# Performance work log

Hardware: AMD Instinct MI355X
Metric: run time of the kernel (lower is better)

## Reference

```python
import jax, jax.numpy as jnp
import numpy as np

EMB_DIM = 32
UID_TGT = 200000
IID_TGT = 50000
BATCH = 128
TOPK = 50000          # hardcoded inside test_source_free branch
TARGET_LABEL = 4.0    # module-level target rating constant


def setup_inputs() -> dict:
    key = jax.random.key(0)
    k1, k2, k3, k4, k5 = jax.random.split(key, 5)
    # x: column 0 = item id (stored as float, like the torch code), cols 1: = src_rate_pre
    iid = jax.random.randint(k1, (BATCH,), 0, IID_TGT).astype(jnp.float32)
    src_rate = jax.random.normal(k2, (BATCH, EMB_DIM), dtype=jnp.float32)
    x = jnp.concatenate([iid[:, None], src_rate], axis=1)  # [B, 1+D]
    uid_weight = 0.1 * jax.random.normal(k3, (UID_TGT, EMB_DIM), dtype=jnp.float32)
    iid_weight = 0.1 * jax.random.normal(k4, (IID_TGT, EMB_DIM), dtype=jnp.float32)
    rp_weight = 0.1 * jax.random.normal(k5, (EMB_DIM, EMB_DIM), dtype=jnp.float32)
    return {"x": x, "uid_weight": uid_weight, "iid_weight": iid_weight, "rp_weight": rp_weight}


def reference(x, uid_weight, iid_weight, rp_weight):
    # === stage == 'test_source_free' ===
    iid = x[:, 0].astype(jnp.int32)                     # [B]
    iid_emb = iid_weight[iid]                           # [B, D] item embedding gather
    src_rate_pre = x[:, 1:] @ rp_weight.T               # [B, D] Linear(emb,emb,bias=False)
    # |uid_emb . src_rate - target|  (torch: [U,B]; here kept [B,U])
    predict_rate = jnp.abs(src_rate_pre @ uid_weight.T - TARGET_LABEL)  # [B, U]
    # torch: full sort ascending + take first TOPK  ==  bottom-TOPK per row
    _, topk_idx = jax.lax.top_k(-predict_rate, TOPK)    # [B, TOPK]
    # voted rating = <selected user emb, item emb>; compute all dots once,
    # then gather (same math as gathering [B,TOPK,D] embeddings and dotting).
    all_scores = iid_emb @ uid_weight.T                 # [B, U]
    voted_rating = jnp.take_along_axis(all_scores, topk_idx, axis=1)  # [B, TOPK]
    mean_rating = jnp.mean(voted_rating, axis=1)        # [B]
    return mean_rating
```

## Files before the change

### kernel.cpp

```cpp
#include <hip/hip_runtime.h>
#include <hip/hip_bf16.h>
#include <stdint.h>

#define EMB    32
#define BATCH  128
#define NU     200000
#define KSEL   50000
#define XCOLS  33
#define SLOTS  64
#define NBLK   256

#define OFF_SPRE   0
#define OFF_IIDE   16384
#define OFF_GHIST  32768
#define OFF_BASE16 163840
#define OFF_PREFIX 164352
#define OFF_M2     164864
#define OFF_EQ     165376
#define OFF_CAND   173568
#define OFF_PART   173568
#define PART_BYTES ((size_t)NBLK * 128 * 256 * 4)

__global__ void prep_kernel(const float* __restrict__ x,
                            const float* __restrict__ iid_w,
                            const float* __restrict__ rp,
                            const float* __restrict__ uid,
                            float* __restrict__ s_pre,
                            float* __restrict__ iid_emb,
                            uint32_t* __restrict__ base16) {
    const int b = blockIdx.x;
    const int t = threadIdx.x;
    __shared__ float xr[EMB];
    if (t < EMB) xr[t] = x[b * XCOLS + 1 + t];
    __syncthreads();
    if (t < EMB) {
        float acc = 0.f;
        #pragma unroll
        for (int k = 0; k < EMB; ++k) acc += xr[k] * rp[t * EMB + k];
        s_pre[b * EMB + t] = acc;
    } else {
        const int d = t - EMB;
        const int iid = (int)x[b * XCOLS];
        iid_emb[b * EMB + d] = iid_w[(size_t)iid * EMB + d];
    }
    __syncthreads();
    if (t == 0) {
        float dot = 0.f;
        #pragma unroll
        for (int k = 0; k < EMB; ++k) dot += s_pre[b * EMB + k] * uid[k];
        const uint32_t bits = __float_as_uint(fabsf(dot - 4.0f));
        const uint32_t hi = bits >> 16;
        base16[b] = (hi > 128u) ? (hi - 128u) : 0u;
    }
}

__global__ void zero_kernel(uint32_t* __restrict__ p, int n) {
    int i = blockIdx.x * blockDim.x + threadIdx.x;
    if (i < n) p[i] = 0u;
}

template <bool PART>
__global__ __launch_bounds__(1024)
__attribute__((amdgpu_waves_per_eu(4, 4)))
void sweep1_kernel(const float* __restrict__ s_pre,
                   const float* __restrict__ uid,
                   const uint32_t* __restrict__ base16,
                   uint32_t* __restrict__ gout,
                   int jchunk) {
    extern __shared__ uint32_t hist[];
    const int t  = threadIdx.x;
    const int b  = t & 127;
    const int jl = t >> 7;
    for (int i = t; i < 128 * 257; i += 1024) hist[i] = 0u;
    float s[EMB];
    #pragma unroll
    for (int d = 0; d < EMB; ++d) s[d] = s_pre[b * EMB + d];
    const uint32_t base = base16[b];
    __syncthreads();

    const int j0 = blockIdx.x * jchunk;
    const int jend = min(j0 + jchunk, NU);
    int j = j0 + jl;
    for (; j + 8 < jend; j += 16) {
        const int ju = __builtin_amdgcn_readfirstlane(j);
        const float* up0 = uid + (size_t)ju * EMB;
        const float* up1 = up0 + 8 * EMB;
        float d0 = 0.f, d1 = 0.f;
        #pragma unroll
        for (int k = 0; k < EMB; ++k) {
            d0 += s[k] * up0[k];
            d1 += s[k] * up1[k];
        }
        const uint32_t bits0 = __float_as_uint(fabsf(d0 - 4.0f));
        const uint32_t bits1 = __float_as_uint(fabsf(d1 - 4.0f));
        int dg0 = (int)(bits0 >> 16) - (int)base; dg0 = dg0 < 0 ? 0 : (dg0 > 255 ? 255 : dg0);
        int dg1 = (int)(bits1 >> 16) - (int)base; dg1 = dg1 < 0 ? 0 : (dg1 > 255 ? 255 : dg1);
        atomicAdd(&hist[b * 257 + dg0], 1u);
        atomicAdd(&hist[b * 257 + dg1], 1u);
    }
    for (; j < jend; j += 8) {
        const int ju = __builtin_amdgcn_readfirstlane(j);
        const float* up0 = uid + (size_t)ju * EMB;
        float d0 = 0.f;
        #pragma unroll
        for (int k = 0; k < EMB; ++k) d0 += s[k] * up0[k];
        const uint32_t bits0 = __float_as_uint(fabsf(d0 - 4.0f));
        int dg0 = (int)(bits0 >> 16) - (int)base; dg0 = dg0 < 0 ? 0 : (dg0 > 255 ? 255 : dg0);
        atomicAdd(&hist[b * 257 + dg0], 1u);
    }
    __syncthreads();
    if (PART) {
        uint32_t* part = gout + (size_t)blockIdx.x * 32768;
        for (int i = t * 4; i < 32768; i += 4096) {
            const int row = i >> 8, d = i & 255;
            uint4 v;
            v.x = hist[row * 257 + d + 0];
            v.y = hist[row * 257 + d + 1];
            v.z = hist[row * 257 + d + 2];
            v.w = hist[row * 257 + d + 3];
            *(uint4*)(part + i) = v;
        }
    } else {
        for (int i = t; i < 128 * 256; i += 1024) {
            const uint32_t c = hist[(i >> 8) * 257 + (i & 255)];
            if (c) atomicAdd(&gout[i], c);
        }
    }
}

__global__ void scan1_kernel(const uint32_t* __restrict__ ghist,
                             const uint32_t* __restrict__ base16,
                             uint32_t* __restrict__ prefix16,
                             uint32_t* __restrict__ m2) {
    const int b = threadIdx.x;
    uint32_t cum = 0, before = 0;
    int c1 = 255;
    for (int d = 0; d < 256; ++d) {
        const uint32_t c = ghist[b * 256 + d];
        if (cum + c >= (uint32_t)KSEL) { c1 = d; before = cum; break; }
        cum += c;
        if (d == 255) before = cum;
    }
    prefix16[b] = base16[b] + (uint32_t)c1;
    m2[b] = (uint32_t)KSEL - before;
}

__global__ __launch_bounds__(256)
void scan1_part_kernel(const uint32_t* __restrict__ part,
                       const uint32_t* __restrict__ base16,
                       uint32_t* __restrict__ prefix16,
                       uint32_t* __restrict__ m2) {
    const int row = blockIdx.x;
    const int t = threadIdx.x;
    __shared__ uint32_t h[256];
    uint32_t a0 = 0, a1 = 0, a2 = 0, a3 = 0;
    const uint32_t* p = part + (size_t)row * 256 + t;
    for (int g = 0; g < NBLK; g += 4) {
        a0 += p[(size_t)(g + 0) * 32768];
        a1 += p[(size_t)(g + 1) * 32768];
        a2 += p[(size_t)(g + 2) * 32768];
        a3 += p[(size_t)(g + 3) * 32768];
    }
    h[t] = a0 + a1 + a2 + a3;
    __syncthreads();
    if (t == 0) {
        uint32_t cum = 0, before = 0; int c1 = 255;
        for (int d = 0; d < 256; ++d) {
            const uint32_t c = h[d];
            if (cum + c >= (uint32_t)KSEL) { c1 = d; before = cum; break; }
            cum += c;
            if (d == 255) before = cum;
        }
        prefix16[row] = base16[row] + (uint32_t)c1;
        m2[row] = (uint32_t)KSEL - before;
    }
}

__global__ __launch_bounds__(1024)
__attribute__((amdgpu_waves_per_eu(4, 4)))
void sweep2_kernel(const float* __restrict__ s_pre,
                   const float* __restrict__ iid_emb,
                   const float* __restrict__ uid,
                   const uint32_t* __restrict__ prefix16,
                   uint32_t* __restrict__ eq_cnt,
                   float* __restrict__ sum_part,
                   uint64_t* __restrict__ cand,
                   int cap, int jchunk) {
    extern __shared__ char smem2[];
    uint64_t* lcand = (uint64_t*)smem2;
    uint32_t* lcnt  = (uint32_t*)(smem2 + 65536);
    uint32_t* lbase = (uint32_t*)(smem2 + 66048);
    float*    sums  = (float*)(smem2 + 66560);
    const int t  = threadIdx.x;
    const int b  = t & 127;
    const int jl = t >> 7;
    if (t < 128) lcnt[t] = 0u;
    float s[EMB], e[EMB];
    #pragma unroll
    for (int d = 0; d < EMB; ++d) { s[d] = s_pre[b*EMB+d]; e[d] = iid_emb[b*EMB+d]; }
    const uint32_t pfx = prefix16[b];
    __syncthreads();

    const int j0 = blockIdx.x * jchunk;
    const int jend = min(j0 + jchunk, NU);
    float local = 0.f;
    int j = j0 + jl;
    for (; j + 8 < jend; j += 16) {
        const int ju = __builtin_amdgcn_readfirstlane(j);
        const float* up0 = uid + (size_t)ju * EMB;
        const float* up1 = up0 + 8 * EMB;
        float d0 = 0.f, v0 = 0.f, d1 = 0.f, v1 = 0.f;
        #pragma unroll
        for (int k = 0; k < EMB; ++k) {
            const float u0 = up0[k], u1 = up1[k];
            d0 += s[k] * u0;  v0 += e[k] * u0;
            d1 += s[k] * u1;  v1 += e[k] * u1;
        }
        const uint32_t bits0 = __float_as_uint(fabsf(d0 - 4.0f));
        const uint32_t bits1 = __float_as_uint(fabsf(d1 - 4.0f));
        const uint32_t hi0 = bits0 >> 16, hi1 = bits1 >> 16;
        local += (hi0 < pfx) ? v0 : 0.f;
        local += (hi1 < pfx) ? v1 : 0.f;
        if (hi0 == pfx) {
            const uint32_t pos = atomicAdd(&lcnt[b], 1u);
            const uint64_t pk = ((uint64_t)bits0 << 32) | (uint32_t)j;
            if (pos < (uint32_t)SLOTS) lcand[b * SLOTS + pos] = pk;
            else {
                const uint32_t g = atomicAdd(&eq_cnt[b * 16], 1u);
                if (g < (uint32_t)cap) cand[(size_t)b * cap + g] = pk;
            }
        }
        if (hi1 == pfx) {
            const uint32_t pos = atomicAdd(&lcnt[b], 1u);
            const uint64_t pk = ((uint64_t)bits1 << 32) | (uint32_t)(j + 8);
            if (pos < (uint32_t)SLOTS) lcand[b * SLOTS + pos] = pk;
            else {
                const uint32_t g = atomicAdd(&eq_cnt[b * 16], 1u);
                if (g < (uint32_t)cap) cand[(size_t)b * cap + g] = pk;
            }
        }
    }
    for (; j < jend; j += 8) {
        const int ju = __builtin_amdgcn_readfirstlane(j);
        const float* up0 = uid + (size_t)ju * EMB;
        float d0 = 0.f, v0 = 0.f;
        #pragma unroll
        for (int k = 0; k < EMB; ++k) {
            const float u0 = up0[k];
            d0 += s[k] * u0;  v0 += e[k] * u0;
        }
        const uint32_t bits0 = __float_as_uint(fabsf(d0 - 4.0f));
        const uint32_t hi0 = bits0 >> 16;
        local += (hi0 < pfx) ? v0 : 0.f;
        if (hi0 == pfx) {
            const uint32_t pos = atomicAdd(&lcnt[b], 1u);
            const uint64_t pk = ((uint64_t)bits0 << 32) | (uint32_t)j;
            if (pos < (uint32_t)SLOTS) lcand[b * SLOTS + pos] = pk;
            else {
                const uint32_t g = atomicAdd(&eq_cnt[b * 16], 1u);
                if (g < (uint32_t)cap) cand[(size_t)b * cap + g] = pk;
            }
        }
    }
    sums[t] = local;
    __syncthreads();
    if (t < 128) {
        float acc = 0.f;
        #pragma unroll
        for (int l = 0; l < 8; ++l) acc += sums[l * 128 + t];
        sum_part[blockIdx.x * 128 + t] = acc;
        const uint32_t n = min(lcnt[t], (uint32_t)SLOTS);
        lbase[t] = atomicAdd(&eq_cnt[t * 16], n);
    }
    __syncthreads();
    for (int i = t; i < 128 * SLOTS; i += 1024) {
        const int bb = i >> 6;
        const int sl = i & 63;
        if (sl < (int)min(lcnt[bb], (uint32_t)SLOTS)) {
            const uint32_t p = lbase[bb] + (uint32_t)sl;
            if (p < (uint32_t)cap) cand[(size_t)bb * cap + p] = lcand[i];
        }
    }
}

__global__ __launch_bounds__(256)
void final_kernel(const float* __restrict__ iid_emb,
                  const float* __restrict__ uid,
                  const uint32_t* __restrict__ m2_,
                  const uint32_t* __restrict__ eq_cnt,
                  const float* __restrict__ sum_part,
                  const uint64_t* __restrict__ cand,
                  int cap, float* __restrict__ out) {
    const int b = blockIdx.x;
    const int t = threadIdx.x;
    __shared__ float red[256];
    __shared__ uint32_t hist[256];
    __shared__ float e[EMB];
    __shared__ uint32_t tie[128];
    __shared__ uint32_t tiecnt, sc2, sm3, sc3, sm4;
    __shared__ float sbelow;
    if (t < EMB) e[t] = iid_emb[b * EMB + t];
    if (t == 0) tiecnt = 0u;
    hist[t] = 0u;
    red[t] = sum_part[t * 128 + b];
    __syncthreads();
    for (int s = 128; s > 0; s >>= 1) { if (t < s) red[t] += red[t + s]; __syncthreads(); }
    if (t == 0) sbelow = red[0];
    __syncthreads();

    const uint32_t ec = eq_cnt[b * 16];
    const int cnt = (int)(ec < (uint32_t)cap ? ec : (uint32_t)cap);
    const uint64_t* cb = cand + (size_t)b * cap;

    for (int i = t; i < cnt; i += 256) {
        const uint32_t low16 = (uint32_t)(cb[i] >> 32) & 0xFFFFu;
        atomicAdd(&hist[low16 >> 8], 1u);
    }
    __syncthreads();
    if (t == 0) {
        const uint32_t m2v = m2_[b];
        uint32_t cum = 0, before = 0; int c2 = 255;
        for (int d = 0; d < 256; ++d) {
            const uint32_t c = hist[d];
            if (cum + c >= m2v) { c2 = d; before = cum; break; }
            cum += c;
        }
        sc2 = (uint32_t)c2; sm3 = m2v - before;
    }
    __syncthreads();
    const uint32_t c2 = sc2;
    hist[t] = 0u;
    __syncthreads();

    for (int i = t; i < cnt; i += 256) {
        const uint32_t low16 = (uint32_t)(cb[i] >> 32) & 0xFFFFu;
        if ((low16 >> 8) == c2) atomicAdd(&hist[low16 & 255u], 1u);
    }
    __syncthreads();
    if (t == 0) {
        const uint32_t m3 = sm3;
        uint32_t cum = 0, before = 0; int c3 = 255;
        for (int d = 0; d < 256; ++d) {
            const uint32_t c = hist[d];
            if (cum + c >= m3) { c3 = d; before = cum; break; }
            cum += c;
        }
        sc3 = (uint32_t)c3; sm4 = m3 - before;
    }
    __syncthreads();
    const uint32_t T16 = (c2 << 8) | sc3;

    float local = 0.f;
    for (int i = t; i < cnt; i += 256) {
        const uint64_t cv = cb[i];
        const uint32_t low16 = (uint32_t)(cv >> 32) & 0xFFFFu;
        if (low16 < T16) {
            const uint32_t j = (uint32_t)cv;
            const float4* u4 = (const float4*)(uid + (size_t)j * EMB);
            float dv = 0.f;
            #pragma unroll
            for (int q = 0; q < 8; ++q) {
                float4 u = u4[q];
                dv += e[4*q+0]*u.x + e[4*q+1]*u.y + e[4*q+2]*u.z + e[4*q+3]*u.w;
            }
            local += dv;
        } else if (low16 == T16) {
            const uint32_t pos = atomicAdd(&tiecnt, 1u);
            if (pos < 128u) tie[pos] = (uint32_t)cv;
        }
    }
    red[t] = local;
    __syncthreads();
    for (int s = 128; s > 0; s >>= 1) { if (t < s) red[t] += red[t + s]; __syncthreads(); }
    if (t == 0) {
        int tc = (int)(tiecnt < 128u ? tiecnt : 128u);
        for (int i = 1; i < tc; ++i) {
            const uint32_t v = tie[i]; int k = i - 1;
            while (k >= 0 && tie[k] > v) { tie[k+1] = tie[k]; --k; }
            tie[k+1] = v;
        }
        const int m4 = (int)sm4;
        float tsum = 0.f;
        for (int i = 0; i < m4 && i < tc; ++i) {
            const uint32_t j = tie[i];
            float dv = 0.f;
            for (int d = 0; d < EMB; ++d) dv += e[d] * uid[(size_t)j * EMB + d];
            tsum += dv;
        }
        out[b] = (sbelow + red[0] + tsum) / (float)KSEL;
    }
}

extern "C" void kernel_launch(void* const* d_in, const int* in_sizes, int n_in,
                              void* d_out, int out_size, void* d_ws, size_t ws_size,
                              hipStream_t stream) {
    const float* x     = (const float*)d_in[0];
    const float* uid   = (const float*)d_in[1];
    const float* iid_w = (const float*)d_in[2];
    const float* rp    = (const float*)d_in[3];
    float* out = (float*)d_out;

    char* ws = (char*)d_ws;
    float*    s_pre    = (float*)(ws + OFF_SPRE);
    float*    iid_emb  = (float*)(ws + OFF_IIDE);
    uint32_t* ghist    = (uint32_t*)(ws + OFF_GHIST);
    float*    sum_part = (float*)(ws + OFF_GHIST);
    uint32_t* base16   = (uint32_t*)(ws + OFF_BASE16);
    uint32_t* prefix16 = (uint32_t*)(ws + OFF_PREFIX);
    uint32_t* m2       = (uint32_t*)(ws + OFF_M2);
    uint32_t* eq_cnt   = (uint32_t*)(ws + OFF_EQ);
    uint32_t* part     = (uint32_t*)(ws + OFF_PART);

    const size_t off_cand2 = OFF_PART + PART_BYTES;
    const bool use_part = ws_size >= off_cand2 + (size_t)128 * 8 * 4096;

    uint64_t* cand;
    int cap;
    if (use_part) {
        cand = (uint64_t*)(ws + off_cand2);
        long long cap_ll = ((long long)ws_size - (long long)off_cand2) / (128LL * 8LL);
        cap = (int)(cap_ll > 16384 ? 16384 : cap_ll);
    } else {
        cand = (uint64_t*)(ws + OFF_CAND);
        long long cap_ll = ((long long)ws_size - OFF_CAND) / (128LL * 8LL);
        cap = (int)(cap_ll > 16384 ? 16384 : (cap_ll < 1 ? 1 : cap_ll));
    }

    {
        const int n = (OFF_CAND - OFF_GHIST) / 4;
        zero_kernel<<<(n + 255) / 256, 256, 0, stream>>>((uint32_t*)(ws + OFF_GHIST), n);
    }
    prep_kernel<<<BATCH, 64, 0, stream>>>(x, iid_w, rp, uid, s_pre, iid_emb, base16);

    const int JC = 782;
    if (use_part) {
        sweep1_kernel<true><<<NBLK, 1024, 128 * 257 * 4, stream>>>(s_pre, uid, base16, part, JC);
        scan1_part_kernel<<<BATCH, 256, 0, stream>>>(part, base16, prefix16, m2);
    } else {
        sweep1_kernel<false><<<NBLK, 1024, 128 * 257 * 4, stream>>>(s_pre, uid, base16, ghist, JC);
        scan1_kernel<<<1, 128, 0, stream>>>(ghist, base16, prefix16, m2);
    }

    sweep2_kernel<<<NBLK, 1024, 65536 + 512 + 512 + 4096, stream>>>(s_pre, iid_emb, uid,
                                                                    prefix16, eq_cnt, sum_part,
                                                                    cand, cap, JC);

    final_kernel<<<BATCH, 256, 0, stream>>>(iid_emb, uid, m2, eq_cnt, sum_part,
                                            cand, cap, out);
}
```

Before: 241.8 us.

## Split each dot product across four lanes with float4 loads and swizzle reductions

Both sweep kernels now give each (batch, user) dot product to four lanes. Each lane loads 8 floats as two float4s and the partial sums are combined with ds_swizzle, replacing per-thread 32-float register arrays and scalar row loads. This cuts register pressure so the fixed waves_per_eu hint can be dropped, and it makes uid reads coalesced vector loads. sweep2 now runs on 512 blocks when the partial-histogram workspace is available, reusing that buffer for sum_part, and the final kernel reduces over a variable number of block partials. Costs include the extra swizzle steps, three of four lanes idling during histogram and candidate updates, and shared-memory atomics for the per-row sums.

```diff
diff --git a/kernel.cpp b/kernel.cpp
--- a/kernel.cpp
+++ b/kernel.cpp
@@ -8,7 +8,8 @@
 #define KSEL   50000
 #define XCOLS  33
 #define SLOTS  64
-#define NBLK   256
+#define NBLK1  256
+#define NBLK2  512
 
 #define OFF_SPRE   0
 #define OFF_IIDE   16384
@@ -19,7 +20,17 @@
 #define OFF_EQ     165376
 #define OFF_CAND   173568
 #define OFF_PART   173568
-#define PART_BYTES ((size_t)NBLK * 128 * 256 * 4)
+#define PART_BYTES ((size_t)NBLK1 * 128 * 256 * 4)
+
+__device__ __forceinline__ float qsum(float x) {
+    x += __int_as_float(__builtin_amdgcn_ds_swizzle(__float_as_int(x), 0x041F));
+    x += __int_as_float(__builtin_amdgcn_ds_swizzle(__float_as_int(x), 0x081F));
+    return x;
+}
+__device__ __forceinline__ float dot8(float4 a0, float4 a1, float4 b0, float4 b1) {
+    return a0.x*b0.x + a0.y*b0.y + a0.z*b0.z + a0.w*b0.w
+         + a1.x*b1.x + a1.y*b1.y + a1.z*b1.z + a1.w*b1.w;
+}
 
 __global__ void prep_kernel(const float* __restrict__ x,
                             const float* __restrict__ iid_w,
@@ -61,52 +72,51 @@
 
 template <bool PART>
 __global__ __launch_bounds__(1024)
-__attribute__((amdgpu_waves_per_eu(4, 4)))
 void sweep1_kernel(const float* __restrict__ s_pre,
                    const float* __restrict__ uid,
                    const uint32_t* __restrict__ base16,
                    uint32_t* __restrict__ gout,
                    int jchunk) {
     extern __shared__ uint32_t hist[];
-    const int t  = threadIdx.x;
-    const int b  = t & 127;
-    const int jl = t >> 7;
+    const int t   = threadIdx.x;
+    const int sub = t & 3;
+    const int gid = t >> 2;
+    const int b   = gid & 127;
+    const int jl  = gid >> 7;
     for (int i = t; i < 128 * 257; i += 1024) hist[i] = 0u;
-    float s[EMB];
-    #pragma unroll
-    for (int d = 0; d < EMB; ++d) s[d] = s_pre[b * EMB + d];
+    const float4* sp = (const float4*)(s_pre + b * EMB + sub * 8);
+    const float4 sa = sp[0], sb = sp[1];
     const uint32_t base = base16[b];
     __syncthreads();
 
     const int j0 = blockIdx.x * jchunk;
     const int jend = min(j0 + jchunk, NU);
     int j = j0 + jl;
-    for (; j + 8 < jend; j += 16) {
-        const int ju = __builtin_amdgcn_readfirstlane(j);
-        const float* up0 = uid + (size_t)ju * EMB;
-        const float* up1 = up0 + 8 * EMB;
-        float d0 = 0.f, d1 = 0.f;
-        #pragma unroll
-        for (int k = 0; k < EMB; ++k) {
-            d0 += s[k] * up0[k];
-            d1 += s[k] * up1[k];
-        }
-        const uint32_t bits0 = __float_as_uint(fabsf(d0 - 4.0f));
-        const uint32_t bits1 = __float_as_uint(fabsf(d1 - 4.0f));
-        int dg0 = (int)(bits0 >> 16) - (int)base; dg0 = dg0 < 0 ? 0 : (dg0 > 255 ? 255 : dg0);
-        int dg1 = (int)(bits1 >> 16) - (int)base; dg1 = dg1 < 0 ? 0 : (dg1 > 255 ? 255 : dg1);
-        atomicAdd(&hist[b * 257 + dg0], 1u);
-        atomicAdd(&hist[b * 257 + dg1], 1u);
-    }
-    for (; j < jend; j += 8) {
-        const int ju = __builtin_amdgcn_readfirstlane(j);
-        const float* up0 = uid + (size_t)ju * EMB;
-        float d0 = 0.f;
-        #pragma unroll
-        for (int k = 0; k < EMB; ++k) d0 += s[k] * up0[k];
-        const uint32_t bits0 = __float_as_uint(fabsf(d0 - 4.0f));
-        int dg0 = (int)(bits0 >> 16) - (int)base; dg0 = dg0 < 0 ? 0 : (dg0 > 255 ? 255 : dg0);
-        atomicAdd(&hist[b * 257 + dg0], 1u);
+    for (; j + 2 < jend; j += 4) {
+        const float4* r0 = (const float4*)(uid + (size_t)j * EMB + sub * 8);
+        const float4* r1 = (const float4*)(uid + (size_t)(j + 2) * EMB + sub * 8);
+        const float4 ua0 = r0[0], ub0 = r0[1];
+        const float4 ua1 = r1[0], ub1 = r1[1];
+        const float d0 = qsum(dot8(sa, sb, ua0, ub0));
+        const float d1 = qsum(dot8(sa, sb, ua1, ub1));
+        if (sub == 0) {
+            const uint32_t bits0 = __float_as_uint(fabsf(d0 - 4.0f));
+            const uint32_t bits1 = __float_as_uint(fabsf(d1 - 4.0f));
+            int dg0 = (int)(bits0 >> 16) - (int)base; dg0 = dg0 < 0 ? 0 : (dg0 > 255 ? 255 : dg0);
+            int dg1 = (int)(bits1 >> 16) - (int)base; dg1 = dg1 < 0 ? 0 : (dg1 > 255 ? 255 : dg1);
+            atomicAdd(&hist[b * 257 + dg0], 1u);
+            atomicAdd(&hist[b * 257 + dg1], 1u);
+        }
+    }
+    for (; j < jend; j += 2) {
+        const float4* r0 = (const float4*)(uid + (size_t)j * EMB + sub * 8);
+        const float4 ua0 = r0[0], ub0 = r0[1];
+        const float d0 = qsum(dot8(sa, sb, ua0, ub0));
+        if (sub == 0) {
+            const uint32_t bits0 = __float_as_uint(fabsf(d0 - 4.0f));
+            int dg0 = (int)(bits0 >> 16) - (int)base; dg0 = dg0 < 0 ? 0 : (dg0 > 255 ? 255 : dg0);
+            atomicAdd(&hist[b * 257 + dg0], 1u);
+        }
     }
     __syncthreads();
     if (PART) {
@@ -155,7 +165,7 @@
     __shared__ uint32_t h[256];
     uint32_t a0 = 0, a1 = 0, a2 = 0, a3 = 0;
     const uint32_t* p = part + (size_t)row * 256 + t;
-    for (int g = 0; g < NBLK; g += 4) {
+    for (int g = 0; g < NBLK1; g += 4) {
         a0 += p[(size_t)(g + 0) * 32768];
         a1 += p[(size_t)(g + 1) * 32768];
         a2 += p[(size_t)(g + 2) * 32768];
@@ -177,7 +187,6 @@
 }
 
 __global__ __launch_bounds__(1024)
-__attribute__((amdgpu_waves_per_eu(4, 4)))
 void sweep2_kernel(const float* __restrict__ s_pre,
                    const float* __restrict__ iid_emb,
                    const float* __restrict__ uid,
@@ -187,17 +196,20 @@
                    uint64_t* __restrict__ cand,
                    int cap, int jchunk) {
     extern __shared__ char smem2[];
-    uint64_t* lcand = (uint64_t*)smem2;
-    uint32_t* lcnt  = (uint32_t*)(smem2 + 65536);
-    uint32_t* lbase = (uint32_t*)(smem2 + 66048);
-    float*    sums  = (float*)(smem2 + 66560);
-    const int t  = threadIdx.x;
-    const int b  = t & 127;
-    const int jl = t >> 7;
-    if (t < 128) lcnt[t] = 0u;
-    float s[EMB], e[EMB];
-    #pragma unroll
-    for (int d = 0; d < EMB; ++d) { s[d] = s_pre[b*EMB+d]; e[d] = iid_emb[b*EMB+d]; }
+    uint64_t* lcand  = (uint64_t*)smem2;
+    uint32_t* lcnt   = (uint32_t*)(smem2 + 65536);
+    uint32_t* lbase  = (uint32_t*)(smem2 + 66048);
+    float*    sums_b = (float*)(smem2 + 66560);
+    const int t   = threadIdx.x;
+    const int sub = t & 3;
+    const int gid = t >> 2;
+    const int b   = gid & 127;
+    const int jl  = gid >> 7;
+    if (t < 128) { lcnt[t] = 0u; sums_b[t] = 0.f; }
+    const float4* sp = (const float4*)(s_pre + b * EMB + sub * 8);
+    const float4 sa = sp[0], sb = sp[1];
+    const float4* ep = (const float4*)(iid_emb + b * EMB + sub * 8);
+    const float4 ea = ep[0], eb = ep[1];
     const uint32_t pfx = prefix16[b];
     __syncthreads();
 
@@ -205,70 +217,65 @@
     const int jend = min(j0 + jchunk, NU);
     float local = 0.f;
     int j = j0 + jl;
-    for (; j + 8 < jend; j += 16) {
-        const int ju = __builtin_amdgcn_readfirstlane(j);
-        const float* up0 = uid + (size_t)ju * EMB;
-        const float* up1 = up0 + 8 * EMB;
-        float d0 = 0.f, v0 = 0.f, d1 = 0.f, v1 = 0.f;
-        #pragma unroll
-        for (int k = 0; k < EMB; ++k) {
-            const float u0 = up0[k], u1 = up1[k];
-            d0 += s[k] * u0;  v0 += e[k] * u0;
-            d1 += s[k] * u1;  v1 += e[k] * u1;
-        }
-        const uint32_t bits0 = __float_as_uint(fabsf(d0 - 4.0f));
-        const uint32_t bits1 = __float_as_uint(fabsf(d1 - 4.0f));
-        const uint32_t hi0 = bits0 >> 16, hi1 = bits1 >> 16;
-        local += (hi0 < pfx) ? v0 : 0.f;
-        local += (hi1 < pfx) ? v1 : 0.f;
-        if (hi0 == pfx) {
-            const uint32_t pos = atomicAdd(&lcnt[b], 1u);
-            const uint64_t pk = ((uint64_t)bits0 << 32) | (uint32_t)j;
-            if (pos < (uint32_t)SLOTS) lcand[b * SLOTS + pos] = pk;
-            else {
-                const uint32_t g = atomicAdd(&eq_cnt[b * 16], 1u);
-                if (g < (uint32_t)cap) cand[(size_t)b * cap + g] = pk;
+    for (; j + 2 < jend; j += 4) {
+        const float4* r0 = (const float4*)(uid + (size_t)j * EMB + sub * 8);
+        const float4* r1 = (const float4*)(uid + (size_t)(j + 2) * EMB + sub * 8);
+        const float4 ua0 = r0[0], ub0 = r0[1];
+        const float4 ua1 = r1[0], ub1 = r1[1];
+        const float d0 = qsum(dot8(sa, sb, ua0, ub0));
+        const float v0 = qsum(dot8(ea, eb, ua0, ub0));
+        const float d1 = qsum(dot8(sa, sb, ua1, ub1));
+        const float v1 = qsum(dot8(ea, eb, ua1, ub1));
+        if (sub == 0) {
+            const uint32_t bits0 = __float_as_uint(fabsf(d0 - 4.0f));
+            const uint32_t bits1 = __float_as_uint(fabsf(d1 - 4.0f));
+            const uint32_t hi0 = bits0 >> 16, hi1 = bits1 >> 16;
+            local += (hi0 < pfx) ? v0 : 0.f;
+            local += (hi1 < pfx) ? v1 : 0.f;
+            if (hi0 == pfx) {
+                const uint32_t pos = atomicAdd(&lcnt[b], 1u);
+                const uint64_t pk = ((uint64_t)bits0 << 32) | (uint32_t)j;
+                if (pos < (uint32_t)SLOTS) lcand[b * SLOTS + pos] = pk;
+                else {
+                    const uint32_t g = atomicAdd(&eq_cnt[b * 16], 1u);
+                    if (g < (uint32_t)cap) cand[(size_t)b * cap + g] = pk;
+                }
             }
-        }
-        if (hi1 == pfx) {
-            const uint32_t pos = atomicAdd(&lcnt[b], 1u);
-            const uint64_t pk = ((uint64_t)bits1 << 32) | (uint32_t)(j + 8);
-            if (pos < (uint32_t)SLOTS) lcand[b * SLOTS + pos] = pk;
-            else {
-                const uint32_t g = atomicAdd(&eq_cnt[b * 16], 1u);
-                if (g < (uint32_t)cap) cand[(size_t)b * cap + g] = pk;
+            if (hi1 == pfx) {
+                const uint32_t pos = atomicAdd(&lcnt[b], 1u);
+                const uint64_t pk = ((uint64_t)bits1 << 32) | (uint32_t)(j + 2);
+                if (pos < (uint32_t)SLOTS) lcand[b * SLOTS + pos] = pk;
+                else {
+                    const uint32_t g = atomicAdd(&eq_cnt[b * 16], 1u);
+                    if (g < (uint32_t)cap) cand[(size_t)b * cap + g] = pk;
+                }
             }
         }
     }
-    for (; j < jend; j += 8) {
-        const int ju = __builtin_amdgcn_readfirstlane(j);
-        const float* up0 = uid + (size_t)ju * EMB;
-        float d0 = 0.f, v0 = 0.f;
-        #pragma unroll
-        for (int k = 0; k < EMB; ++k) {
-            const float u0 = up0[k];
-            d0 += s[k] * u0;  v0 += e[k] * u0;
-        }
-        const uint32_t bits0 = __float_as_uint(fabsf(d0 - 4.0f));
-        const uint32_t hi0 = bits0 >> 16;
-        local += (hi0 < pfx) ? v0 : 0.f;
-        if (hi0 == pfx) {
-            const uint32_t pos = atomicAdd(&lcnt[b], 1u);
-            const uint64_t pk = ((uint64_t)bits0 << 32) | (uint32_t)j;
-            if (pos < (uint32_t)SLOTS) lcand[b * SLOTS + pos] = pk;
-            else {
-                const uint32_t g = atomicAdd(&eq_cnt[b * 16], 1u);
-                if (g < (uint32_t)cap) cand[(size_t)b * cap + g] = pk;
+    for (; j < jend; j += 2) {
+        const float4* r0 = (const float4*)(uid + (size_t)j * EMB + sub * 8);
+        const float4 ua0 = r0[0], ub0 = r0[1];
+        const float d0 = qsum(dot8(sa, sb, ua0, ub0));
+        const float v0 = qsum(dot8(ea, eb, ua0, ub0));
+        if (sub == 0) {
+            const uint32_t bits0 = __float_as_uint(fabsf(d0 - 4.0f));
+            const uint32_t hi0 = bits0 >> 16;
+            local += (hi0 < pfx) ? v0 : 0.f;
+            if (hi0 == pfx) {
+                const uint32_t pos = atomicAdd(&lcnt[b], 1u);
+                const uint64_t pk = ((uint64_t)bits0 << 32) | (uint32_t)j;
+                if (pos < (uint32_t)SLOTS) lcand[b * SLOTS + pos] = pk;
+                else {
+                    const uint32_t g = atomicAdd(&eq_cnt[b * 16], 1u);
+                    if (g < (uint32_t)cap) cand[(size_t)b * cap + g] = pk;
+                }
             }
         }
     }
-    sums[t] = local;
+    if (sub == 0 && local != 0.f) atomicAdd(&sums_b[b], local);
     __syncthreads();
     if (t < 128) {
-        float acc = 0.f;
-        #pragma unroll
-        for (int l = 0; l < 8; ++l) acc += sums[l * 128 + t];
-        sum_part[blockIdx.x * 128 + t] = acc;
+        sum_part[(size_t)blockIdx.x * 128 + t] = sums_b[t];
         const uint32_t n = min(lcnt[t], (uint32_t)SLOTS);
         lbase[t] = atomicAdd(&eq_cnt[t * 16], n);
     }
@@ -290,7 +297,7 @@
                   const uint32_t* __restrict__ eq_cnt,
                   const float* __restrict__ sum_part,
                   const uint64_t* __restrict__ cand,
-                  int cap, float* __restrict__ out) {
+                  int cap, int g2, float* __restrict__ out) {
     const int b = blockIdx.x;
     const int t = threadIdx.x;
     __shared__ float red[256];
@@ -302,7 +309,11 @@
     if (t < EMB) e[t] = iid_emb[b * EMB + t];
     if (t == 0) tiecnt = 0u;
     hist[t] = 0u;
-    red[t] = sum_part[t * 128 + b];
+    {
+        float acc = 0.f;
+        for (int g = t; g < g2; g += 256) acc += sum_part[(size_t)g * 128 + b];
+        red[t] = acc;
+    }
     __syncthreads();
     for (int s = 128; s > 0; s >>= 1) { if (t < s) red[t] += red[t + s]; __syncthreads(); }
     if (t == 0) sbelow = red[0];
@@ -404,7 +415,6 @@
     float*    s_pre    = (float*)(ws + OFF_SPRE);
     float*    iid_emb  = (float*)(ws + OFF_IIDE);
     uint32_t* ghist    = (uint32_t*)(ws + OFF_GHIST);
-    float*    sum_part = (float*)(ws + OFF_GHIST);
     uint32_t* base16   = (uint32_t*)(ws + OFF_BASE16);
     uint32_t* prefix16 = (uint32_t*)(ws + OFF_PREFIX);
     uint32_t* m2       = (uint32_t*)(ws + OFF_M2);
@@ -416,15 +426,22 @@
 
     uint64_t* cand;
     int cap;
+    float* sum_part;
+    int G2, JC2;
     if (use_part) {
         cand = (uint64_t*)(ws + off_cand2);
         long long cap_ll = ((long long)ws_size - (long long)off_cand2) / (128LL * 8LL);
         cap = (int)(cap_ll > 16384 ? 16384 : cap_ll);
+        sum_part = (float*)part;
+        G2 = NBLK2;
     } else {
         cand = (uint64_t*)(ws + OFF_CAND);
         long long cap_ll = ((long long)ws_size - OFF_CAND) / (128LL * 8LL);
         cap = (int)(cap_ll > 16384 ? 16384 : (cap_ll < 1 ? 1 : cap_ll));
-    }
+        sum_part = (float*)(ws + OFF_GHIST);
+        G2 = NBLK1;
+    }
+    JC2 = (NU + G2 - 1) / G2;
 
     {
         const int n = (OFF_CAND - OFF_GHIST) / 4;
@@ -432,19 +449,19 @@
     }
     prep_kernel<<<BATCH, 64, 0, stream>>>(x, iid_w, rp, uid, s_pre, iid_emb, base16);
 
-    const int JC = 782;
+    const int JC1 = (NU + NBLK1 - 1) / NBLK1;
     if (use_part) {
-        sweep1_kernel<true><<<NBLK, 1024, 128 * 257 * 4, stream>>>(s_pre, uid, base16, part, JC);
+        sweep1_kernel<true><<<NBLK1, 1024, 128 * 257 * 4, stream>>>(s_pre, uid, base16, part, JC1);
         scan1_part_kernel<<<BATCH, 256, 0, stream>>>(part, base16, prefix16, m2);
     } else {
-        sweep1_kernel<false><<<NBLK, 1024, 128 * 257 * 4, stream>>>(s_pre, uid, base16, ghist, JC);
+        sweep1_kernel<false><<<NBLK1, 1024, 128 * 257 * 4, stream>>>(s_pre, uid, base16, ghist, JC1);
         scan1_kernel<<<1, 128, 0, stream>>>(ghist, base16, prefix16, m2);
     }
 
-    sweep2_kernel<<<NBLK, 1024, 65536 + 512 + 512 + 4096, stream>>>(s_pre, iid_emb, uid,
-                                                                    prefix16, eq_cnt, sum_part,
-                                                                    cand, cap, JC);
+    sweep2_kernel<<<G2, 1024, 65536 + 512 + 512 + 512, stream>>>(s_pre, iid_emb, uid,
+                                                                 prefix16, eq_cnt, sum_part,
+                                                                 cand, cap, JC2);
 
     final_kernel<<<BATCH, 256, 0, stream>>>(iid_emb, uid, m2, eq_cnt, sum_part,
-                                            cand, cap, out);
-}
+                                            cand, cap, G2, out);
+}
```

Result: slower. 305.5 us (+26.4%).

## Pack 16-bit histograms, split sweep2 dot products across lane pairs, double grid

Applied to the files above, without the earlier changes.

The first sweep's shared histograms now pack two 16-bit bins per word, halving LDS use, and runs on twice as many blocks without the fixed waves-per-EU attribute. The second sweep splits the two dot products (selection score and item score) across adjacent lanes, keeping one 32-float vector per thread instead of two, and exchanges the results with a DPP swap. Partial sums are reduced with LDS atomics. The zero kernel is dropped on the partials path, with eq_cnt cleared in prep instead. The aim is higher occupancy and more parallelism, at the cost of half the lanes idling during selection logic and more partial histograms for the scan to read.

```diff
diff --git a/kernel.cpp b/kernel.cpp
--- a/kernel.cpp
+++ b/kernel.cpp
@@ -8,7 +8,10 @@
 #define KSEL   50000
 #define XCOLS  33
 #define SLOTS  64
-#define NBLK   256
+#define G1     512
+#define G2P    512
+#define G2F    256
+#define HISTW  (128 * 129)
 
 #define OFF_SPRE   0
 #define OFF_IIDE   16384
@@ -19,7 +22,12 @@
 #define OFF_EQ     165376
 #define OFF_CAND   173568
 #define OFF_PART   173568
-#define PART_BYTES ((size_t)NBLK * 128 * 256 * 4)
+#define PART_BYTES ((size_t)G1 * HISTW * 4)
+
+__device__ __forceinline__ float xor1(float x) {
+    int r = __builtin_amdgcn_update_dpp(0, __float_as_int(x), 0xB1, 0xF, 0xF, true);
+    return __int_as_float(r);
+}
 
 __global__ void prep_kernel(const float* __restrict__ x,
                             const float* __restrict__ iid_w,
@@ -27,11 +35,13 @@
                             const float* __restrict__ uid,
                             float* __restrict__ s_pre,
                             float* __restrict__ iid_emb,
-                            uint32_t* __restrict__ base16) {
+                            uint32_t* __restrict__ base16,
+                            uint32_t* __restrict__ eq_cnt) {
     const int b = blockIdx.x;
     const int t = threadIdx.x;
     __shared__ float xr[EMB];
     if (t < EMB) xr[t] = x[b * XCOLS + 1 + t];
+    if (t == 63) eq_cnt[b * 16] = 0u;
     __syncthreads();
     if (t < EMB) {
         float acc = 0.f;
@@ -61,7 +71,6 @@
 
 template <bool PART>
 __global__ __launch_bounds__(1024)
-__attribute__((amdgpu_waves_per_eu(4, 4)))
 void sweep1_kernel(const float* __restrict__ s_pre,
                    const float* __restrict__ uid,
                    const uint32_t* __restrict__ base16,
@@ -71,7 +80,7 @@
     const int t  = threadIdx.x;
     const int b  = t & 127;
     const int jl = t >> 7;
-    for (int i = t; i < 128 * 257; i += 1024) hist[i] = 0u;
+    for (int i = t; i < HISTW; i += 1024) hist[i] = 0u;
     float s[EMB];
     #pragma unroll
     for (int d = 0; d < EMB; ++d) s[d] = s_pre[b * EMB + d];
@@ -95,8 +104,8 @@
         const uint32_t bits1 = __float_as_uint(fabsf(d1 - 4.0f));
         int dg0 = (int)(bits0 >> 16) - (int)base; dg0 = dg0 < 0 ? 0 : (dg0 > 255 ? 255 : dg0);
         int dg1 = (int)(bits1 >> 16) - (int)base; dg1 = dg1 < 0 ? 0 : (dg1 > 255 ? 255 : dg1);
-        atomicAdd(&hist[b * 257 + dg0], 1u);
-        atomicAdd(&hist[b * 257 + dg1], 1u);
+        atomicAdd(&hist[b * 129 + (dg0 >> 1)], 1u << ((dg0 & 1) * 16));
+        atomicAdd(&hist[b * 129 + (dg1 >> 1)], 1u << ((dg1 & 1) * 16));
     }
     for (; j < jend; j += 8) {
         const int ju = __builtin_amdgcn_readfirstlane(j);
@@ -106,23 +115,16 @@
         for (int k = 0; k < EMB; ++k) d0 += s[k] * up0[k];
         const uint32_t bits0 = __float_as_uint(fabsf(d0 - 4.0f));
         int dg0 = (int)(bits0 >> 16) - (int)base; dg0 = dg0 < 0 ? 0 : (dg0 > 255 ? 255 : dg0);
-        atomicAdd(&hist[b * 257 + dg0], 1u);
+        atomicAdd(&hist[b * 129 + (dg0 >> 1)], 1u << ((dg0 & 1) * 16));
     }
     __syncthreads();
     if (PART) {
-        uint32_t* part = gout + (size_t)blockIdx.x * 32768;
-        for (int i = t * 4; i < 32768; i += 4096) {
-            const int row = i >> 8, d = i & 255;
-            uint4 v;
-            v.x = hist[row * 257 + d + 0];
-            v.y = hist[row * 257 + d + 1];
-            v.z = hist[row * 257 + d + 2];
-            v.w = hist[row * 257 + d + 3];
-            *(uint4*)(part + i) = v;
-        }
+        uint32_t* part = gout + (size_t)blockIdx.x * HISTW;
+        for (int i = t; i < HISTW; i += 1024) part[i] = hist[i];
     } else {
         for (int i = t; i < 128 * 256; i += 1024) {
-            const uint32_t c = hist[(i >> 8) * 257 + (i & 255)];
+            const int r = i >> 8, d = i & 255;
+            const uint32_t c = (hist[r * 129 + (d >> 1)] >> ((d & 1) * 16)) & 0xFFFFu;
             if (c) atomicAdd(&gout[i], c);
         }
     }
@@ -153,13 +155,14 @@
     const int row = blockIdx.x;
     const int t = threadIdx.x;
     __shared__ uint32_t h[256];
+    const int sh = (t & 1) * 16;
+    const uint32_t* p = part + (size_t)row * 129 + (t >> 1);
     uint32_t a0 = 0, a1 = 0, a2 = 0, a3 = 0;
-    const uint32_t* p = part + (size_t)row * 256 + t;
-    for (int g = 0; g < NBLK; g += 4) {
-        a0 += p[(size_t)(g + 0) * 32768];
-        a1 += p[(size_t)(g + 1) * 32768];
-        a2 += p[(size_t)(g + 2) * 32768];
-        a3 += p[(size_t)(g + 3) * 32768];
+    for (int g = 0; g < G1; g += 4) {
+        a0 += (p[(size_t)(g + 0) * HISTW] >> sh) & 0xFFFFu;
+        a1 += (p[(size_t)(g + 1) * HISTW] >> sh) & 0xFFFFu;
+        a2 += (p[(size_t)(g + 2) * HISTW] >> sh) & 0xFFFFu;
+        a3 += (p[(size_t)(g + 3) * HISTW] >> sh) & 0xFFFFu;
     }
     h[t] = a0 + a1 + a2 + a3;
     __syncthreads();
@@ -177,7 +180,6 @@
 }
 
 __global__ __launch_bounds__(1024)
-__attribute__((amdgpu_waves_per_eu(4, 4)))
 void sweep2_kernel(const float* __restrict__ s_pre,
                    const float* __restrict__ iid_emb,
                    const float* __restrict__ uid,
@@ -187,17 +189,25 @@
                    uint64_t* __restrict__ cand,
                    int cap, int jchunk) {
     extern __shared__ char smem2[];
-    uint64_t* lcand = (uint64_t*)smem2;
-    uint32_t* lcnt  = (uint32_t*)(smem2 + 65536);
-    uint32_t* lbase = (uint32_t*)(smem2 + 66048);
-    float*    sums  = (float*)(smem2 + 66560);
-    const int t  = threadIdx.x;
-    const int b  = t & 127;
-    const int jl = t >> 7;
-    if (t < 128) lcnt[t] = 0u;
-    float s[EMB], e[EMB];
-    #pragma unroll
-    for (int d = 0; d < EMB; ++d) { s[d] = s_pre[b*EMB+d]; e[d] = iid_emb[b*EMB+d]; }
+    uint64_t* lcand  = (uint64_t*)smem2;
+    uint32_t* lcnt   = (uint32_t*)(smem2 + 65536);
+    uint32_t* lbase  = (uint32_t*)(smem2 + 66048);
+    float*    sums_b = (float*)(smem2 + 66560);
+    const int t   = threadIdx.x;
+    const int par = t & 1;
+    const int pr  = t >> 1;
+    const int b   = pr & 127;
+    const int jl  = pr >> 7;
+    if (t < 128) { lcnt[t] = 0u; sums_b[t] = 0.f; }
+    float c[EMB];
+    {
+        const float4* cp4 = (const float4*)((par ? iid_emb : s_pre) + b * EMB);
+        #pragma unroll
+        for (int q = 0; q < 8; ++q) {
+            float4 v = cp4[q];
+            c[4*q+0] = v.x; c[4*q+1] = v.y; c[4*q+2] = v.z; c[4*q+3] = v.w;
+        }
+    }
     const uint32_t pfx = prefix16[b];
     __syncthreads();
 
@@ -205,70 +215,70 @@
     const int jend = min(j0 + jchunk, NU);
     float local = 0.f;
     int j = j0 + jl;
-    for (; j + 8 < jend; j += 16) {
+    for (; j + 4 < jend; j += 8) {
         const int ju = __builtin_amdgcn_readfirstlane(j);
         const float* up0 = uid + (size_t)ju * EMB;
-        const float* up1 = up0 + 8 * EMB;
-        float d0 = 0.f, v0 = 0.f, d1 = 0.f, v1 = 0.f;
+        const float* up1 = up0 + 4 * EMB;
+        float a0 = 0.f, a1 = 0.f;
         #pragma unroll
         for (int k = 0; k < EMB; ++k) {
-            const float u0 = up0[k], u1 = up1[k];
-            d0 += s[k] * u0;  v0 += e[k] * u0;
-            d1 += s[k] * u1;  v1 += e[k] * u1;
-        }
-        const uint32_t bits0 = __float_as_uint(fabsf(d0 - 4.0f));
-        const uint32_t bits1 = __float_as_uint(fabsf(d1 - 4.0f));
-        const uint32_t hi0 = bits0 >> 16, hi1 = bits1 >> 16;
-        local += (hi0 < pfx) ? v0 : 0.f;
-        local += (hi1 < pfx) ? v1 : 0.f;
-        if (hi0 == pfx) {
-            const uint32_t pos = atomicAdd(&lcnt[b], 1u);
-            const uint64_t pk = ((uint64_t)bits0 << 32) | (uint32_t)j;
-            if (pos < (uint32_t)SLOTS) lcand[b * SLOTS + pos] = pk;
-            else {
-                const uint32_t g = atomicAdd(&eq_cnt[b * 16], 1u);
-                if (g < (uint32_t)cap) cand[(size_t)b * cap + g] = pk;
+            a0 += c[k] * up0[k];
+            a1 += c[k] * up1[k];
+        }
+        const float p0 = xor1(a0);
+        const float p1 = xor1(a1);
+        if (par == 0) {
+            const uint32_t bits0 = __float_as_uint(fabsf(a0 - 4.0f));
+            const uint32_t bits1 = __float_as_uint(fabsf(a1 - 4.0f));
+            const uint32_t hi0 = bits0 >> 16, hi1 = bits1 >> 16;
+            local += (hi0 < pfx) ? p0 : 0.f;
+            local += (hi1 < pfx) ? p1 : 0.f;
+            if (hi0 == pfx) {
+                const uint32_t pos = atomicAdd(&lcnt[b], 1u);
+                const uint64_t pk = ((uint64_t)bits0 << 32) | (uint32_t)j;
+                if (pos < (uint32_t)SLOTS) lcand[b * SLOTS + pos] = pk;
+                else {
+                    const uint32_t g = atomicAdd(&eq_cnt[b * 16], 1u);
+                    if (g < (uint32_t)cap) cand[(size_t)b * cap + g] = pk;
+                }
             }
-        }
-        if (hi1 == pfx) {
-            const uint32_t pos = atomicAdd(&lcnt[b], 1u);
-            const uint64_t pk = ((uint64_t)bits1 << 32) | (uint32_t)(j + 8);
-            if (pos < (uint32_t)SLOTS) lcand[b * SLOTS + pos] = pk;
-            else {
-                const uint32_t g = atomicAdd(&eq_cnt[b * 16], 1u);
-                if (g < (uint32_t)cap) cand[(size_t)b * cap + g] = pk;
+            if (hi1 == pfx) {
+                const uint32_t pos = atomicAdd(&lcnt[b], 1u);
+                const uint64_t pk = ((uint64_t)bits1 << 32) | (uint32_t)(j + 4);
+                if (pos < (uint32_t)SLOTS) lcand[b * SLOTS + pos] = pk;
+                else {
+                    const uint32_t g = atomicAdd(&eq_cnt[b * 16], 1u);
+                    if (g < (uint32_t)cap) cand[(size_t)b * cap + g] = pk;
+                }
             }
         }
     }
-    for (; j < jend; j += 8) {
+    for (; j < jend; j += 4) {
         const int ju = __builtin_amdgcn_readfirstlane(j);
         const float* up0 = uid + (size_t)ju * EMB;
-        float d0 = 0.f, v0 = 0.f;
-        #pragma unroll
-        for (int k = 0; k < EMB; ++k) {
-            const float u0 = up0[k];
-            d0 += s[k] * u0;  v0 += e[k] * u0;
-        }
-        const uint32_t bits0 = __float_as_uint(fabsf(d0 - 4.0f));
-        const uint32_t hi0 = bits0 >> 16;
-        local += (hi0 < pfx) ? v0 : 0.f;
-        if (hi0 == pfx) {
-            const uint32_t pos = atomicAdd(&lcnt[b], 1u);
-            const uint64_t pk = ((uint64_t)bits0 << 32) | (uint32_t)j;
-            if (pos < (uint32_t)SLOTS) lcand[b * SLOTS + pos] = pk;
-            else {
-                const uint32_t g = atomicAdd(&eq_cnt[b * 16], 1u);
-                if (g < (uint32_t)cap) cand[(size_t)b * cap + g] = pk;
+        float a0 = 0.f;
+        #pragma unroll
+        for (int k = 0; k < EMB; ++k) a0 += c[k] * up0[k];
+        const float p0 = xor1(a0);
+        if (par == 0) {
+            const uint32_t bits0 = __float_as_uint(fabsf(a0 - 4.0f));
+            const uint32_t hi0 = bits0 >> 16;
+            local += (hi0 < pfx) ? p0 : 0.f;
+            if (hi0 == pfx) {
+                const uint32_t pos = atomicAdd(&lcnt[b], 1u);
+                const uint64_t pk = ((uint64_t)bits0 << 32) | (uint32_t)j;
+                if (pos < (uint32_t)SLOTS) lcand[b * SLOTS + pos] = pk;
+                else {
+                    const uint32_t g = atomicAdd(&eq_cnt[b * 16], 1u);
+                    if (g < (uint32_t)cap) cand[(size_t)b * cap + g] = pk;
+                }
             }
         }
     }
-    sums[t] = local;
+    if (par == 0 && local != 0.f) atomicAdd(&sums_b[b], local);
     __syncthreads();
     if (t < 128) {
-        float acc = 0.f;
-        #pragma unroll
-        for (int l = 0; l < 8; ++l) acc += sums[l * 128 + t];
-        sum_part[blockIdx.x * 128 + t] = acc;
+        sum_part[(size_t)blockIdx.x * 128 + t] = sums_b[t];
         const uint32_t n = min(lcnt[t], (uint32_t)SLOTS);
         lbase[t] = atomicAdd(&eq_cnt[t * 16], n);
     }
@@ -290,7 +300,7 @@
                   const uint32_t* __restrict__ eq_cnt,
                   const float* __restrict__ sum_part,
                   const uint64_t* __restrict__ cand,
-                  int cap, float* __restrict__ out) {
+                  int cap, int g2, float* __restrict__ out) {
     const int b = blockIdx.x;
     const int t = threadIdx.x;
     __shared__ float red[256];
@@ -302,7 +312,11 @@
     if (t < EMB) e[t] = iid_emb[b * EMB + t];
     if (t == 0) tiecnt = 0u;
     hist[t] = 0u;
-    red[t] = sum_part[t * 128 + b];
+    {
+        float acc = 0.f;
+        for (int g = t; g < g2; g += 256) acc += sum_part[(size_t)g * 128 + b];
+        red[t] = acc;
+    }
     __syncthreads();
     for (int s = 128; s > 0; s >>= 1) { if (t < s) red[t] += red[t + s]; __syncthreads(); }
     if (t == 0) sbelow = red[0];
@@ -404,7 +418,6 @@
     float*    s_pre    = (float*)(ws + OFF_SPRE);
     float*    iid_emb  = (float*)(ws + OFF_IIDE);
     uint32_t* ghist    = (uint32_t*)(ws + OFF_GHIST);
-    float*    sum_part = (float*)(ws + OFF_GHIST);
     uint32_t* base16   = (uint32_t*)(ws + OFF_BASE16);
     uint32_t* prefix16 = (uint32_t*)(ws + OFF_PREFIX);
     uint32_t* m2       = (uint32_t*)(ws + OFF_M2);
@@ -416,35 +429,40 @@
 
     uint64_t* cand;
     int cap;
+    float* sum_part;
+    int g2;
     if (use_part) {
         cand = (uint64_t*)(ws + off_cand2);
         long long cap_ll = ((long long)ws_size - (long long)off_cand2) / (128LL * 8LL);
         cap = (int)(cap_ll > 16384 ? 16384 : cap_ll);
+        sum_part = (float*)part;
+        g2 = G2P;
     } else {
         cand = (uint64_t*)(ws + OFF_CAND);
         long long cap_ll = ((long long)ws_size - OFF_CAND) / (128LL * 8LL);
         cap = (int)(cap_ll > 16384 ? 16384 : (cap_ll < 1 ? 1 : cap_ll));
-    }
-
-    {
+        sum_part = (float*)(ws + OFF_GHIST);
+        g2 = G2F;
         const int n = (OFF_CAND - OFF_GHIST) / 4;
         zero_kernel<<<(n + 255) / 256, 256, 0, stream>>>((uint32_t*)(ws + OFF_GHIST), n);
     }
-    prep_kernel<<<BATCH, 64, 0, stream>>>(x, iid_w, rp, uid, s_pre, iid_emb, base16);
-
-    const int JC = 782;
+
+    prep_kernel<<<BATCH, 64, 0, stream>>>(x, iid_w, rp, uid, s_pre, iid_emb, base16, eq_cnt);
+
+    const int jc1 = (NU + G1 - 1) / G1;
     if (use_part) {
-        sweep1_kernel<true><<<NBLK, 1024, 128 * 257 * 4, stream>>>(s_pre, uid, base16, part, JC);
+        sweep1_kernel<true><<<G1, 1024, HISTW * 4, stream>>>(s_pre, uid, base16, part, jc1);
         scan1_part_kernel<<<BATCH, 256, 0, stream>>>(part, base16, prefix16, m2);
     } else {
-        sweep1_kernel<false><<<NBLK, 1024, 128 * 257 * 4, stream>>>(s_pre, uid, base16, ghist, JC);
+        sweep1_kernel<false><<<G1, 1024, HISTW * 4, stream>>>(s_pre, uid, base16, ghist, jc1);
         scan1_kernel<<<1, 128, 0, stream>>>(ghist, base16, prefix16, m2);
     }
 
-    sweep2_kernel<<<NBLK, 1024, 65536 + 512 + 512 + 4096, stream>>>(s_pre, iid_emb, uid,
-                                                                    prefix16, eq_cnt, sum_part,
-                                                                    cand, cap, JC);
+    const int jc2 = (NU + g2 - 1) / g2;
+    sweep2_kernel<<<g2, 1024, 65536 + 1536, stream>>>(s_pre, iid_emb, uid,
+                                                      prefix16, eq_cnt, sum_part,
+                                                      cand, cap, jc2);
 
     final_kernel<<<BATCH, 256, 0, stream>>>(iid_emb, uid, m2, eq_cnt, sum_part,
-                                            cand, cap, out);
-}
+                                            cand, cap, g2, out);
+}
```

New measurement: 248.4 us. +2.7%, slower.
